# Kernel tuning notes

Measured on AMD Instinct MI355X. Metric: run time of the kernel, lower is better.

Reference implementation:

```python
import jax, jax.numpy as jnp
import numpy as np

N, F, T, C = 20000, 4, 12, 256
HID, OUT = 128, 12
ER, E = 30000, 320000


def _gcn_agg(xw, src, dst, w):
    """GCNConv propagation with self-loops (weight 1): D^-1/2 (A+I) D^-1/2 @ xw.
    xw: [N, T, C] pre-projected features; src/dst: [E] int; w: [E] edge weights."""
    n = xw.shape[0]
    deg = jnp.zeros((n,), xw.dtype).at[dst].add(w) + 1.0  # +1 from self-loop
    dinv = jax.lax.rsqrt(deg)
    coef = (dinv[src] * w * dinv[dst])[:, None, None]      # [E,1,1]
    out = jnp.zeros_like(xw).at[dst].add(coef * xw[src])   # scatter-add messages
    return out + (dinv * dinv)[:, None, None] * xw         # self-loop term


def _regional_conv(x, Wc, bc, regs):
    # Shared GCNConv applied to each of the 5 state graphs, outputs summed.
    xw = jnp.einsum("nft,fc->ntc", x, Wc)  # [N, T, C], all periods at once
    out = bc
    for (src, dst, w) in regs:
        out = out + _gcn_agg(xw, src, dst, w)
    return out


def _forward(x, attrs, idxs, Wc_z, bc_z, Wl_z, bl_z, Wc_h, bc_h, Wl_h, bl_h,
             attention, W1, b1, W2, b2):
    regs = [(idx[0], idx[1], w) for idx, w in zip(idxs, attrs)]
    # A3TGCN runs an independent TGCN-GRU step per period from H=None (zeros),
    # then attention-averages over periods. With H=0:
    #   Z = sigmoid(linear_z([conv_z(X_t), 0]))   (hidden half of Wl drops out)
    #   reset gate R multiplies H=0, so it has no effect on the output
    #   H_tilde = tanh(linear_h([conv_h(X_t), 0]));  H_t = (1-Z)*H_tilde
    cz = _regional_conv(x, Wc_z, bc_z, regs)         # [N, T, C]
    Z = jax.nn.sigmoid(cz @ Wl_z[:C] + bl_z)
    ch = _regional_conv(x, Wc_h, bc_h, regs)
    Htilde = jnp.tanh(ch @ Wl_h[:C] + bl_h)
    Ht = (1.0 - Z) * Htilde                          # [N, T, C]
    probs = jax.nn.softmax(attention)                # [T]
    h = jnp.einsum("ntc,t->nc", Ht, probs)           # temporal attention pooling
    y = jax.nn.relu(h)
    y = jax.nn.relu(y @ W1 + b1)
    y = y @ W2 + b2
    return y, h


def setup_inputs():
    key = jax.random.key(0)
    ks = jax.random.split(key, 32)
    s = 0.05
    inp = {
        "x": jax.random.normal(ks[0], (N, F, T), jnp.float32),
        "edge_index": jax.random.randint(ks[1], (2, E), 0, N, jnp.int32),
    }
    regions = ["IA", "KS", "KY", "OH", "WI"]
    for i, nm in enumerate(regions):
        inp[nm + "edge_index"] = jax.random.randint(ks[2 + i], (2, ER), 0, N, jnp.int32)
    for i, nm in enumerate(regions):
        inp[nm + "edge_attr"] = jax.random.uniform(ks[7 + i], (ER,), jnp.float32)
    for gi, g in enumerate(["z", "r", "h"]):
        inp["Wc_" + g] = jax.random.normal(ks[12 + gi], (F, C), jnp.float32) * s
        inp["bc_" + g] = jnp.zeros((C,), jnp.float32)
        inp["Wl_" + g] = jax.random.normal(ks[15 + gi], (2 * C, C), jnp.float32) * s
        inp["bl_" + g] = jnp.zeros((C,), jnp.float32)
    inp["attention"] = jax.random.normal(ks[18], (T,), jnp.float32)
    inp["W1"] = jax.random.normal(ks[19], (C, HID), jnp.float32) * s
    inp["b1"] = jnp.zeros((HID,), jnp.float32)
    inp["W2"] = jax.random.normal(ks[20], (HID, OUT), jnp.float32) * s
    inp["b2"] = jnp.zeros((OUT,), jnp.float32)
    return inp


def reference(x, edge_index, IAedge_index, KSedge_index, KYedge_index, OHedge_index, WIedge_index,
              IAedge_attr, KSedge_attr, KYedge_attr, OHedge_attr, WIedge_attr,
              Wc_z, bc_z, Wl_z, bl_z, Wc_r, bc_r, Wl_r, bl_r, Wc_h, bc_h, Wl_h, bl_h,
              attention, W1, b1, W2, b2):
    # The full-graph edge_index and the reset-gate parameters are carried by the
    # original module but cannot influence the output (regional convs use the 5
    # state graphs; the reset gate multiplies the zero initial hidden state).
    idxs = [IAedge_index, KSedge_index, KYedge_index, OHedge_index, WIedge_index]
    attrs = [IAedge_attr, KSedge_attr, KYedge_attr, OHedge_attr, WIedge_attr]
    return _forward(x, attrs, idxs, Wc_z, bc_z, Wl_z, bl_z, Wc_h, bc_h, Wl_h, bl_h,
                    attention, W1, b1, W2, b2)
```

## Files before the change

### kernel.cpp

```cpp
#include <hip/hip_runtime.h>

constexpr int N    = 20000;
constexpr int T    = 12;
constexpr int C    = 256;
constexpr int HIDN = 128;
constexpr int OUTD = 12;
constexpr int ER   = 30000;
constexpr int NFT  = 48;
constexpr int EDGE_TOT = 5 * ER;
constexpr int CAP      = 32;
constexpr int EB       = 586;

constexpr int WS_DEG    = 0;
constexpr int WS_CNT    = 100000;
constexpr int WS_MV     = 120000;
constexpr int WS_ZEND   = 122576;
constexpr int WS_WP     = 122576;
constexpr int WS_W2T    = 138960;
constexpr int WS_BUCKET = 140496;

constexpr float LOG2E = 1.4426950408889634f;

typedef __attribute__((ext_vector_type(8))) short short8;
typedef __attribute__((ext_vector_type(4))) float floatx4;
typedef __attribute__((ext_vector_type(2))) float floatx2;

#if __has_builtin(__builtin_amdgcn_exp2f)
#define EXP2(x) __builtin_amdgcn_exp2f(x)
#else
#define EXP2(x) exp2f(x)
#endif

__device__ __forceinline__ floatx2 pk_fma(floatx2 a, floatx2 b, floatx2 c) {
  floatx2 r;
  r.x = fmaf(a.x, b.x, c.x);
  r.y = fmaf(a.y, b.y, c.y);
  return r;
}

__device__ __forceinline__ short f2bf(float f) {
  unsigned u = __float_as_uint(f);
  u = u + 0x7fffu + ((u >> 16) & 1u);
  return (short)(u >> 16);
}

__device__ __forceinline__ void pick_region(
    int r,
    const int* e0, const int* e1, const int* e2, const int* e3, const int* e4,
    const float* a0, const float* a1, const float* a2, const float* a3, const float* a4,
    const int*& ei, const float*& ea) {
  switch (r) {
    case 0: ei = e0; ea = a0; break;
    case 1: ei = e1; ea = a1; break;
    case 2: ei = e2; ea = a2; break;
    case 3: ei = e3; ea = a3; break;
    default: ei = e4; ea = a4; break;
  }
}

__global__ void k_prep(
    const float* __restrict__ Wc_z, const float* __restrict__ bc_z,
    const float* __restrict__ Wl_z, const float* __restrict__ bl_z,
    const float* __restrict__ Wc_h, const float* __restrict__ bc_h,
    const float* __restrict__ Wl_h, const float* __restrict__ bl_h,
    const float* __restrict__ att, const float* __restrict__ W1,
    const float* __restrict__ W2,
    const int* __restrict__ e0, const int* __restrict__ e1,
    const int* __restrict__ e2, const int* __restrict__ e3,
    const int* __restrict__ e4,
    const float* __restrict__ a0, const float* __restrict__ a1,
    const float* __restrict__ a2, const float* __restrict__ a3,
    const float* __restrict__ a4,
    float* __restrict__ Mv, short* __restrict__ Wp, float* __restrict__ W2t,
    float* __restrict__ deg, int* __restrict__ cnt, int2* __restrict__ bucket) {
  int b = blockIdx.x, tid = threadIdx.x;
  if (b < 16) {
    int g  = b >> 3;
    int ch = b & 7;
    int k  = tid;
    const float* Wc = g ? Wc_h : Wc_z;
    const float* bc = g ? bc_h : bc_z;
    const float* Wl = g ? Wl_h : Wl_z;
    const float* bl = g ? bl_h : bl_z;
    float scale = g ? 2.0f * LOG2E : LOG2E;
    float m0 = 0.f, m1 = 0.f, m2 = 0.f, m3 = 0.f;
    float v = (ch == 0) ? bl[k] : 0.0f;
    int c0 = ch * 32;
    for (int c = c0; c < c0 + 32; c++) {
      float wl = Wl[c * C + k];
      m0 = fmaf(Wc[0 * C + c], wl, m0);
      m1 = fmaf(Wc[1 * C + c], wl, m1);
      m2 = fmaf(Wc[2 * C + c], wl, m2);
      m3 = fmaf(Wc[3 * C + c], wl, m3);
      v  = fmaf(bc[c], wl, v);
    }
    float* o = Mv + g * (5 * C);
    atomicAdd(&o[0 * C + k], scale * m0);
    atomicAdd(&o[1 * C + k], scale * m1);
    atomicAdd(&o[2 * C + k], scale * m2);
    atomicAdd(&o[3 * C + k], scale * m3);
    atomicAdd(&o[4 * C + k], scale * v);
    return;
  }
  if (b == 16) {
    if (tid < T) {
      float amax = -3.0e38f;
      for (int t = 0; t < T; t++) amax = fmaxf(amax, att[t]);
      float s = 0.f;
      for (int t = 0; t < T; t++) s += __expf(att[t] - amax);
      Mv[10 * C + tid] = __expf(att[tid] - amax) / s;
    }
    return;
  }
  if (b < 152) {
    int idx = (b - 17) * 256 + tid;
    if (idx < 32768) {
      int j    = idx & 7;
      int lane = (idx >> 3) & 63;
      int ch   = (idx >> 9) & 7;
      int kt   = idx >> 12;
      int cin  = ch * 32 + (lane >> 4) * 8 + j;
      int kout = kt * 16 + (lane & 15);
      Wp[idx] = f2bf(W1[cin * HIDN + kout]);
    } else if (idx < 32768 + 1536) {
      int r = idx - 32768;
      int o = r >> 7, k = r & 127;
      W2t[r] = W2[k * OUTD + o];
    }
    return;
  }
  int i = (b - 152) * 256 + tid;
  if (i >= EDGE_TOT) return;
  int r = i / ER;
  int e = i - r * ER;
  const int* ei; const float* ea;
  pick_region(r, e0, e1, e2, e3, e4, a0, a1, a2, a3, a4, ei, ea);
  int src = ei[e];
  int dst = ei[ER + e];
  float w = ea[e];
  atomicAdd(&deg[r * N + dst], w);
  int slot = atomicAdd(&cnt[dst], 1);
  if (slot < CAP) bucket[dst * CAP + slot] = make_int2(src | (r << 15), __float_as_int(w));
}

__global__ __launch_bounds__(256) void k_fused(
    const float* __restrict__ x, const float* __restrict__ deg,
    const int* __restrict__ cnt, const int2* __restrict__ bucket,
    const float* __restrict__ Mv, const short* __restrict__ Wp,
    const float* __restrict__ b1, const float* __restrict__ W2t,
    const float* __restrict__ b2,
    float* __restrict__ y_out, float* __restrict__ h_out) {
  __shared__ float xs[16][NFT];
  __shared__ short hs[16][264];
  __shared__ float y1s[16][132];
  int tid = threadIdx.x;
  int wave = tid >> 6, lane = tid & 63;
  int n0 = blockIdx.x * 16;

  {
    int q = lane < NFT ? lane : NFT - 1;
    int sl = lane & (CAP - 1);
    int nb = n0 + wave * 4;
    int4 cv4 = *(const int4*)&cnt[nb];
    int cvs[4] = {cv4.x, cv4.y, cv4.z, cv4.w};
    int2 mrs[4];
#pragma unroll
    for (int nl = 0; nl < 4; nl++) mrs[nl] = bucket[(nb + nl) * CAP + sl];

#pragma unroll
    for (int nl = 0; nl < 4; nl++) {
      int rl = wave * 4 + nl;
      int n = nb + nl;
      float dd0 = rsqrtf(deg[0 * N + n] + 1.0f);
      float dd1 = rsqrtf(deg[1 * N + n] + 1.0f);
      float dd2 = rsqrtf(deg[2 * N + n] + 1.0f);
      float dd3 = rsqrtf(deg[3 * N + n] + 1.0f);
      float dd4 = rsqrtf(deg[4 * N + n] + 1.0f);
      float s = dd0 * dd0 + dd1 * dd1 + dd2 * dd2 + dd3 * dd3 + dd4 * dd4;
      float facc = s * x[n * NFT + q];

      int cv = cvs[nl];
      if (cv > CAP) cv = CAP;
      int2 m  = mrs[nl];
      bool valid = sl < cv;
      int key  = valid ? m.x : 0;
      int srcv = key & 0x7fff;
      int rr   = key >> 15;
      float dsrc = deg[rr * N + srcv];
      float ddn = rr == 0 ? dd0 : rr == 1 ? dd1 : rr == 2 ? dd2
                : rr == 3 ? dd3 : dd4;
      float cf = valid ? rsqrtf(dsrc + 1.0f) * __int_as_float(m.y) * ddn : 0.0f;

      float f1 = 0.f, f2 = 0.f, f3 = 0.f;
      int cvr = (cv + 3) & ~3;
      for (int j = 0; j < cvr; j += 4) {
        int s0 = __shfl(srcv, j);
        int s1 = __shfl(srcv, j + 1);
        int s2 = __shfl(srcv, j + 2);
        int s3 = __shfl(srcv, j + 3);
        float c0 = __shfl(cf, j);
        float c1 = __shfl(cf, j + 1);
        float c2 = __shfl(cf, j + 2);
        float c3 = __shfl(cf, j + 3);
        float x0 = x[s0 * NFT + q];
        float x1 = x[s1 * NFT + q];
        float x2 = x[s2 * NFT + q];
        float x3 = x[s3 * NFT + q];
        facc = fmaf(c0, x0, facc);
        f1 = fmaf(c1, x1, f1);
        f2 = fmaf(c2, x2, f2);
        f3 = fmaf(c3, x3, f3);
      }
      facc = (facc + f1) + (f2 + f3);
      if (lane < NFT) xs[rl][lane] = facc;
    }
  }
  __syncthreads();

  {
    int half = wave & 1;
    int nb   = (wave >> 1) * 8;
    int c0 = half * 128 + (lane << 1);
    const float* Mz = Mv;
    const float* Mh = Mv + 5 * C;
    floatx2 mz[4], mh[4], vz, vh;
#pragma unroll
    for (int f = 0; f < 4; f++) {
      mz[f] = *(const floatx2*)(Mz + f * C + c0);
      mh[f] = *(const floatx2*)(Mh + f * C + c0);
    }
    vz = *(const floatx2*)(Mz + 4 * C + c0);
    vh = *(const floatx2*)(Mh + 4 * C + c0);

#pragma unroll
    for (int nl = 0; nl < 8; nl++) {
      int rl = nb + nl;
      int n = n0 + rl;
      const float* xr = &xs[rl][0];
      floatx2 acc = {0.f, 0.f};
#pragma unroll
      for (int tb = 0; tb < 3; tb++) {
        float4 xf0 = *(const float4*)(xr + 0 * T + tb * 4);
        float4 xf1 = *(const float4*)(xr + 1 * T + tb * 4);
        float4 xf2 = *(const float4*)(xr + 2 * T + tb * 4);
        float4 xf3 = *(const float4*)(xr + 3 * T + tb * 4);
        float xs0[4] = {xf0.x, xf0.y, xf0.z, xf0.w};
        float xs1[4] = {xf1.x, xf1.y, xf1.z, xf1.w};
        float xs2[4] = {xf2.x, xf2.y, xf2.z, xf2.w};
        float xs3[4] = {xf3.x, xf3.y, xf3.z, xf3.w};
#pragma unroll
        for (int tt = 0; tt < 4; tt++) {
          int t = tb * 4 + tt;
          float p = Mv[10 * C + t];
          floatx2 x0 = {xs0[tt], xs0[tt]};
          floatx2 x1 = {xs1[tt], xs1[tt]};
          floatx2 x2 = {xs2[tt], xs2[tt]};
          floatx2 x3 = {xs3[tt], xs3[tt]};
          floatx2 az = pk_fma(mz[0], x0, pk_fma(mz[1], x1, pk_fma(mz[2], x2, pk_fma(mz[3], x3, vz))));
          floatx2 ah = pk_fma(mh[0], x0, pk_fma(mh[1], x1, pk_fma(mh[2], x2, pk_fma(mh[3], x3, vh))));
          floatx2 e1, e2;
          e1.x = EXP2(az.x); e1.y = EXP2(az.y);
          e2.x = EXP2(ah.x); e2.y = EXP2(ah.y);
          floatx2 one = {1.f, 1.f};
          floatx2 d1 = e1 + one;
          floatx2 d2 = e2 + one;
          floatx2 rD;
          rD.x = __builtin_amdgcn_rcpf(d1.x * d2.x);
          rD.y = __builtin_amdgcn_rcpf(d1.y * d2.y);
          floatx2 pv = {p, p};
          floatx2 pn = pk_fma(pv, e2, -pv);
          acc = pk_fma(pn, rD, acc);
        }
      }
      float2 o = {acc.x, acc.y};
      *(float2*)(h_out + n * C + c0) = o;
      unsigned pk = (unsigned short)f2bf(fmaxf(acc.x, 0.f)) |
                    ((unsigned)(unsigned short)f2bf(fmaxf(acc.y, 0.f)) << 16);
      *(unsigned*)&hs[rl][c0] = pk;
    }
  }
  __syncthreads();

  {
    int quad = lane >> 4, col = lane & 15;
    floatx4 acc2[2];
    acc2[0] = {0.f, 0.f, 0.f, 0.f};
    acc2[1] = {0.f, 0.f, 0.f, 0.f};
#pragma unroll
    for (int ch = 0; ch < 8; ch++) {
      short8 a = *(const short8*)&hs[col][ch * 32 + quad * 8];
#pragma unroll
      for (int kk = 0; kk < 2; kk++) {
        short8 bb = ((const short8*)Wp)[((wave * 2 + kk) * 8 + ch) * 64 + lane];
        acc2[kk] = __builtin_amdgcn_mfma_f32_16x16x32_bf16(a, bb, acc2[kk], 0, 0, 0);
      }
    }
#pragma unroll
    for (int kk = 0; kk < 2; kk++) {
      int kt = wave * 2 + kk;
      float bias = b1[kt * 16 + col];
#pragma unroll
      for (int r = 0; r < 4; r++)
        y1s[quad * 4 + r][kt * 16 + col] = fmaxf(acc2[kk][r] + bias, 0.f);
    }
  }
  __syncthreads();

  if (tid < 16 * OUTD) {
    int nl = tid / OUTD, o = tid - nl * OUTD;
    float sacc = b2[o];
    const float* yr = &y1s[nl][0];
    const float* wr = W2t + o * HIDN;
#pragma unroll 8
    for (int k4 = 0; k4 < 32; k4++) {
      float4 yv = *(const float4*)(yr + 4 * k4);
      float4 wv = *(const float4*)(wr + 4 * k4);
      sacc = fmaf(yv.x, wv.x, fmaf(yv.y, wv.y, fmaf(yv.z, wv.z, fmaf(yv.w, wv.w, sacc))));
    }
    y_out[(n0 + nl) * OUTD + o] = sacc;
  }
}

extern "C" void kernel_launch(void* const* d_in, const int* in_sizes, int n_in,
                              void* d_out, int out_size, void* d_ws, size_t ws_size,
                              hipStream_t stream) {
  const float* x   = (const float*)d_in[0];
  const int* eIA = (const int*)d_in[2];
  const int* eKS = (const int*)d_in[3];
  const int* eKY = (const int*)d_in[4];
  const int* eOH = (const int*)d_in[5];
  const int* eWI = (const int*)d_in[6];
  const float* aIA = (const float*)d_in[7];
  const float* aKS = (const float*)d_in[8];
  const float* aKY = (const float*)d_in[9];
  const float* aOH = (const float*)d_in[10];
  const float* aWI = (const float*)d_in[11];
  const float* Wc_z = (const float*)d_in[12];
  const float* bc_z = (const float*)d_in[13];
  const float* Wl_z = (const float*)d_in[14];
  const float* bl_z = (const float*)d_in[15];
  const float* Wc_h = (const float*)d_in[20];
  const float* bc_h = (const float*)d_in[21];
  const float* Wl_h = (const float*)d_in[22];
  const float* bl_h = (const float*)d_in[23];
  const float* att  = (const float*)d_in[24];
  const float* W1   = (const float*)d_in[25];
  const float* b1   = (const float*)d_in[26];
  const float* W2   = (const float*)d_in[27];
  const float* b2   = (const float*)d_in[28];

  float* ws     = (float*)d_ws;
  float* deg    = ws + WS_DEG;
  int*   cnt    = (int*)(ws + WS_CNT);
  float* Mv     = ws + WS_MV;
  short* Wp     = (short*)(ws + WS_WP);
  float* W2t    = ws + WS_W2T;
  int2*  bucket = (int2*)(ws + WS_BUCKET);

  float* y_out = (float*)d_out;
  float* h_out = y_out + N * OUTD;

  hipMemsetAsync(deg, 0, WS_ZEND * sizeof(float), stream);

  k_prep<<<152 + EB, 256, 0, stream>>>(Wc_z, bc_z, Wl_z, bl_z,
                                       Wc_h, bc_h, Wl_h, bl_h,
                                       att, W1, W2,
                                       eIA, eKS, eKY, eOH, eWI,
                                       aIA, aKS, aKY, aOH, aWI,
                                       Mv, Wp, W2t, deg, cnt, bucket);
  k_fused<<<N / 16, 256, 0, stream>>>(x, deg, cnt, bucket, Mv, Wp, b1, W2t, b2,
                                      y_out, h_out);
}
```

Before: 180.1 us.

## Merge memset, prep and fused kernels into one persistent kernel with grid barriers

Replaces the memset plus two kernel launches with a single persistent kernel of 1024 blocks. Blocks zero the workspace, hit a software grid barrier, run the prep work, hit a second barrier, then loop over node tiles. The gather loop is also reworked to interleave the four nodes of each wave, with readfirstlane on the neighbour counts, to expose more memory parallelism. This removes launch gaps and kernel boundaries at the cost of spin-wait barriers, which assume all 1024 blocks are co-resident, and fewer blocks for the main phase.

```diff
diff --git a/kernel.cpp b/kernel.cpp
--- a/kernel.cpp
+++ b/kernel.cpp
@@ -10,6 +10,9 @@
 constexpr int EDGE_TOT = 5 * ER;
 constexpr int CAP      = 32;
 constexpr int EB       = 586;
+constexpr int PREP_B   = 152 + EB;
+constexpr int NT       = N / 16;
+constexpr int GRID     = 1024;
 
 constexpr int WS_DEG    = 0;
 constexpr int WS_CNT    = 100000;
@@ -58,7 +61,22 @@
   }
 }
 
-__global__ void k_prep(
+__device__ unsigned g_bar[2];
+
+__device__ __forceinline__ void grid_barrier(int which) {
+  __syncthreads();
+  if (threadIdx.x == 0) {
+    unsigned v = __hip_atomic_fetch_add(&g_bar[which], 1u,
+                                        __ATOMIC_ACQ_REL, __HIP_MEMORY_SCOPE_AGENT);
+    unsigned target = (v & ~(unsigned)(GRID - 1)) + (unsigned)GRID;
+    while (__hip_atomic_load(&g_bar[which], __ATOMIC_ACQUIRE,
+                             __HIP_MEMORY_SCOPE_AGENT) < target)
+      __builtin_amdgcn_s_sleep(1);
+  }
+  __syncthreads();
+}
+
+__global__ __launch_bounds__(256, 4) void k_all(
     const float* __restrict__ Wc_z, const float* __restrict__ bc_z,
     const float* __restrict__ Wl_z, const float* __restrict__ bl_z,
     const float* __restrict__ Wc_h, const float* __restrict__ bc_h,
@@ -71,9 +89,23 @@
     const float* __restrict__ a0, const float* __restrict__ a1,
     const float* __restrict__ a2, const float* __restrict__ a3,
     const float* __restrict__ a4,
+    const float* __restrict__ x, const float* __restrict__ b1,
+    const float* __restrict__ b2,
     float* __restrict__ Mv, short* __restrict__ Wp, float* __restrict__ W2t,
-    float* __restrict__ deg, int* __restrict__ cnt, int2* __restrict__ bucket) {
+    float* __restrict__ deg, int* __restrict__ cnt, int2* __restrict__ bucket,
+    float* __restrict__ y_out, float* __restrict__ h_out) {
+  __shared__ float xs[16][NFT];
+  __shared__ short hs[16][264];
+  __shared__ float y1s[16][132];
+
   int b = blockIdx.x, tid = threadIdx.x;
+
+  {
+    int gz = b * 256 + tid;
+    if (gz < WS_ZEND) deg[gz] = 0.0f;
+  }
+  grid_barrier(0);
+
   if (b < 16) {
     int g  = b >> 3;
     int ch = b & 7;
@@ -100,9 +132,7 @@
     atomicAdd(&o[2 * C + k], scale * m2);
     atomicAdd(&o[3 * C + k], scale * m3);
     atomicAdd(&o[4 * C + k], scale * v);
-    return;
-  }
-  if (b == 16) {
+  } else if (b == 16) {
     if (tid < T) {
       float amax = -3.0e38f;
       for (int t = 0; t < T; t++) amax = fmaxf(amax, att[t]);
@@ -110,9 +140,7 @@
       for (int t = 0; t < T; t++) s += __expf(att[t] - amax);
       Mv[10 * C + tid] = __expf(att[tid] - amax) / s;
     }
-    return;
-  }
-  if (b < 152) {
+  } else if (b < 152) {
     int idx = (b - 17) * 256 + tid;
     if (idx < 32768) {
       int j    = idx & 7;
@@ -127,197 +155,211 @@
       int o = r >> 7, k = r & 127;
       W2t[r] = W2[k * OUTD + o];
     }
-    return;
+  } else if (b < PREP_B) {
+    int i = (b - 152) * 256 + tid;
+    if (i < EDGE_TOT) {
+      int r = i / ER;
+      int e = i - r * ER;
+      const int* ei; const float* ea;
+      pick_region(r, e0, e1, e2, e3, e4, a0, a1, a2, a3, a4, ei, ea);
+      int src = ei[e];
+      int dst = ei[ER + e];
+      float w = ea[e];
+      atomicAdd(&deg[r * N + dst], w);
+      int slot = atomicAdd(&cnt[dst], 1);
+      if (slot < CAP) bucket[dst * CAP + slot] = make_int2(src | (r << 15), __float_as_int(w));
+    }
   }
-  int i = (b - 152) * 256 + tid;
-  if (i >= EDGE_TOT) return;
-  int r = i / ER;
-  int e = i - r * ER;
-  const int* ei; const float* ea;
-  pick_region(r, e0, e1, e2, e3, e4, a0, a1, a2, a3, a4, ei, ea);
-  int src = ei[e];
-  int dst = ei[ER + e];
-  float w = ea[e];
-  atomicAdd(&deg[r * N + dst], w);
-  int slot = atomicAdd(&cnt[dst], 1);
-  if (slot < CAP) bucket[dst * CAP + slot] = make_int2(src | (r << 15), __float_as_int(w));
-}
-
-__global__ __launch_bounds__(256) void k_fused(
-    const float* __restrict__ x, const float* __restrict__ deg,
-    const int* __restrict__ cnt, const int2* __restrict__ bucket,
-    const float* __restrict__ Mv, const short* __restrict__ Wp,
-    const float* __restrict__ b1, const float* __restrict__ W2t,
-    const float* __restrict__ b2,
-    float* __restrict__ y_out, float* __restrict__ h_out) {
-  __shared__ float xs[16][NFT];
-  __shared__ short hs[16][264];
-  __shared__ float y1s[16][132];
-  int tid = threadIdx.x;
+  grid_barrier(1);
+
   int wave = tid >> 6, lane = tid & 63;
-  int n0 = blockIdx.x * 16;
-
-  {
-    int q = lane < NFT ? lane : NFT - 1;
-    int sl = lane & (CAP - 1);
-    int nb = n0 + wave * 4;
-    int4 cv4 = *(const int4*)&cnt[nb];
-    int cvs[4] = {cv4.x, cv4.y, cv4.z, cv4.w};
-    int2 mrs[4];
-#pragma unroll
-    for (int nl = 0; nl < 4; nl++) mrs[nl] = bucket[(nb + nl) * CAP + sl];
-
-#pragma unroll
-    for (int nl = 0; nl < 4; nl++) {
-      int rl = wave * 4 + nl;
-      int n = nb + nl;
-      float dd0 = rsqrtf(deg[0 * N + n] + 1.0f);
-      float dd1 = rsqrtf(deg[1 * N + n] + 1.0f);
-      float dd2 = rsqrtf(deg[2 * N + n] + 1.0f);
-      float dd3 = rsqrtf(deg[3 * N + n] + 1.0f);
-      float dd4 = rsqrtf(deg[4 * N + n] + 1.0f);
-      float s = dd0 * dd0 + dd1 * dd1 + dd2 * dd2 + dd3 * dd3 + dd4 * dd4;
-      float facc = s * x[n * NFT + q];
-
-      int cv = cvs[nl];
-      if (cv > CAP) cv = CAP;
-      int2 m  = mrs[nl];
-      bool valid = sl < cv;
-      int key  = valid ? m.x : 0;
-      int srcv = key & 0x7fff;
-      int rr   = key >> 15;
-      float dsrc = deg[rr * N + srcv];
-      float ddn = rr == 0 ? dd0 : rr == 1 ? dd1 : rr == 2 ? dd2
-                : rr == 3 ? dd3 : dd4;
-      float cf = valid ? rsqrtf(dsrc + 1.0f) * __int_as_float(m.y) * ddn : 0.0f;
-
-      float f1 = 0.f, f2 = 0.f, f3 = 0.f;
-      int cvr = (cv + 3) & ~3;
-      for (int j = 0; j < cvr; j += 4) {
-        int s0 = __shfl(srcv, j);
-        int s1 = __shfl(srcv, j + 1);
-        int s2 = __shfl(srcv, j + 2);
-        int s3 = __shfl(srcv, j + 3);
-        float c0 = __shfl(cf, j);
-        float c1 = __shfl(cf, j + 1);
-        float c2 = __shfl(cf, j + 2);
-        float c3 = __shfl(cf, j + 3);
-        float x0 = x[s0 * NFT + q];
-        float x1 = x[s1 * NFT + q];
-        float x2 = x[s2 * NFT + q];
-        float x3 = x[s3 * NFT + q];
-        facc = fmaf(c0, x0, facc);
-        f1 = fmaf(c1, x1, f1);
-        f2 = fmaf(c2, x2, f2);
-        f3 = fmaf(c3, x3, f3);
-      }
-      facc = (facc + f1) + (f2 + f3);
-      if (lane < NFT) xs[rl][lane] = facc;
-    }
-  }
-  __syncthreads();
-
-  {
-    int half = wave & 1;
-    int nb   = (wave >> 1) * 8;
-    int c0 = half * 128 + (lane << 1);
-    const float* Mz = Mv;
-    const float* Mh = Mv + 5 * C;
-    floatx2 mz[4], mh[4], vz, vh;
-#pragma unroll
-    for (int f = 0; f < 4; f++) {
-      mz[f] = *(const floatx2*)(Mz + f * C + c0);
-      mh[f] = *(const floatx2*)(Mh + f * C + c0);
-    }
-    vz = *(const floatx2*)(Mz + 4 * C + c0);
-    vh = *(const floatx2*)(Mh + 4 * C + c0);
-
-#pragma unroll
-    for (int nl = 0; nl < 8; nl++) {
-      int rl = nb + nl;
-      int n = n0 + rl;
-      const float* xr = &xs[rl][0];
-      floatx2 acc = {0.f, 0.f};
-#pragma unroll
-      for (int tb = 0; tb < 3; tb++) {
-        float4 xf0 = *(const float4*)(xr + 0 * T + tb * 4);
-        float4 xf1 = *(const float4*)(xr + 1 * T + tb * 4);
-        float4 xf2 = *(const float4*)(xr + 2 * T + tb * 4);
-        float4 xf3 = *(const float4*)(xr + 3 * T + tb * 4);
-        float xs0[4] = {xf0.x, xf0.y, xf0.z, xf0.w};
-        float xs1[4] = {xf1.x, xf1.y, xf1.z, xf1.w};
-        float xs2[4] = {xf2.x, xf2.y, xf2.z, xf2.w};
-        float xs3[4] = {xf3.x, xf3.y, xf3.z, xf3.w};
-#pragma unroll
-        for (int tt = 0; tt < 4; tt++) {
-          int t = tb * 4 + tt;
-          float p = Mv[10 * C + t];
-          floatx2 x0 = {xs0[tt], xs0[tt]};
-          floatx2 x1 = {xs1[tt], xs1[tt]};
-          floatx2 x2 = {xs2[tt], xs2[tt]};
-          floatx2 x3 = {xs3[tt], xs3[tt]};
-          floatx2 az = pk_fma(mz[0], x0, pk_fma(mz[1], x1, pk_fma(mz[2], x2, pk_fma(mz[3], x3, vz))));
-          floatx2 ah = pk_fma(mh[0], x0, pk_fma(mh[1], x1, pk_fma(mh[2], x2, pk_fma(mh[3], x3, vh))));
-          floatx2 e1, e2;
-          e1.x = EXP2(az.x); e1.y = EXP2(az.y);
-          e2.x = EXP2(ah.x); e2.y = EXP2(ah.y);
-          floatx2 one = {1.f, 1.f};
-          floatx2 d1 = e1 + one;
-          floatx2 d2 = e2 + one;
-          floatx2 rD;
-          rD.x = __builtin_amdgcn_rcpf(d1.x * d2.x);
-          rD.y = __builtin_amdgcn_rcpf(d1.y * d2.y);
-          floatx2 pv = {p, p};
-          floatx2 pn = pk_fma(pv, e2, -pv);
-          acc = pk_fma(pn, rD, acc);
+
+  for (int tile = b; tile < NT; tile += GRID) {
+    int n0 = tile * 16;
+
+    {
+      int q = lane < NFT ? lane : NFT - 1;
+      int sl = lane & (CAP - 1);
+      int nb = n0 + wave * 4;
+      int4 cv4 = *(const int4*)&cnt[nb];
+      int cvs[4];
+      cvs[0] = __builtin_amdgcn_readfirstlane(cv4.x);
+      cvs[1] = __builtin_amdgcn_readfirstlane(cv4.y);
+      cvs[2] = __builtin_amdgcn_readfirstlane(cv4.z);
+      cvs[3] = __builtin_amdgcn_readfirstlane(cv4.w);
+#pragma unroll
+      for (int nl = 0; nl < 4; nl++) cvs[nl] = cvs[nl] > CAP ? CAP : cvs[nl];
+
+      int2 mrs[4];
+#pragma unroll
+      for (int nl = 0; nl < 4; nl++) mrs[nl] = bucket[(nb + nl) * CAP + sl];
+
+      int srcs[4]; float cfs[4];
+      float fa[4], fb[4], fc[4], fd[4];
+#pragma unroll
+      for (int nl = 0; nl < 4; nl++) {
+        int n = nb + nl;
+        float dd0 = rsqrtf(deg[0 * N + n] + 1.0f);
+        float dd1 = rsqrtf(deg[1 * N + n] + 1.0f);
+        float dd2 = rsqrtf(deg[2 * N + n] + 1.0f);
+        float dd3 = rsqrtf(deg[3 * N + n] + 1.0f);
+        float dd4 = rsqrtf(deg[4 * N + n] + 1.0f);
+        float s = dd0 * dd0 + dd1 * dd1 + dd2 * dd2 + dd3 * dd3 + dd4 * dd4;
+        fa[nl] = s * x[n * NFT + q];
+        fb[nl] = 0.f; fc[nl] = 0.f; fd[nl] = 0.f;
+
+        bool valid = sl < cvs[nl];
+        int key  = valid ? mrs[nl].x : 0;
+        int srcv = key & 0x7fff;
+        int rr   = key >> 15;
+        float dsrc = deg[rr * N + srcv];
+        float ddn = rr == 0 ? dd0 : rr == 1 ? dd1 : rr == 2 ? dd2
+                  : rr == 3 ? dd3 : dd4;
+        cfs[nl]  = valid ? rsqrtf(dsrc + 1.0f) * __int_as_float(mrs[nl].y) * ddn : 0.0f;
+        srcs[nl] = srcv;
+      }
+
+      int cvr0 = (cvs[0] + 3) & ~3, cvr1 = (cvs[1] + 3) & ~3;
+      int cvr2 = (cvs[2] + 3) & ~3, cvr3 = (cvs[3] + 3) & ~3;
+      int cvm01 = cvr0 > cvr1 ? cvr0 : cvr1;
+      int cvm23 = cvr2 > cvr3 ? cvr2 : cvr3;
+      int cvm = cvm01 > cvm23 ? cvm01 : cvm23;
+      int cvr[4] = {cvr0, cvr1, cvr2, cvr3};
+
+      for (int j = 0; j < cvm; j += 4) {
+#pragma unroll
+        for (int nl = 0; nl < 4; nl++) {
+          if (j < cvr[nl]) {
+            int s0 = __shfl(srcs[nl], j);
+            int s1 = __shfl(srcs[nl], j + 1);
+            int s2 = __shfl(srcs[nl], j + 2);
+            int s3 = __shfl(srcs[nl], j + 3);
+            float c0 = __shfl(cfs[nl], j);
+            float c1 = __shfl(cfs[nl], j + 1);
+            float c2 = __shfl(cfs[nl], j + 2);
+            float c3 = __shfl(cfs[nl], j + 3);
+            float x0 = x[s0 * NFT + q];
+            float x1 = x[s1 * NFT + q];
+            float x2 = x[s2 * NFT + q];
+            float x3 = x[s3 * NFT + q];
+            fa[nl] = fmaf(c0, x0, fa[nl]);
+            fb[nl] = fmaf(c1, x1, fb[nl]);
+            fc[nl] = fmaf(c2, x2, fc[nl]);
+            fd[nl] = fmaf(c3, x3, fd[nl]);
+          }
         }
       }
-      float2 o = {acc.x, acc.y};
-      *(float2*)(h_out + n * C + c0) = o;
-      unsigned pk = (unsigned short)f2bf(fmaxf(acc.x, 0.f)) |
-                    ((unsigned)(unsigned short)f2bf(fmaxf(acc.y, 0.f)) << 16);
-      *(unsigned*)&hs[rl][c0] = pk;
-    }
-  }
-  __syncthreads();
-
-  {
-    int quad = lane >> 4, col = lane & 15;
-    floatx4 acc2[2];
-    acc2[0] = {0.f, 0.f, 0.f, 0.f};
-    acc2[1] = {0.f, 0.f, 0.f, 0.f};
-#pragma unroll
-    for (int ch = 0; ch < 8; ch++) {
-      short8 a = *(const short8*)&hs[col][ch * 32 + quad * 8];
+#pragma unroll
+      for (int nl = 0; nl < 4; nl++) {
+        float facc = (fa[nl] + fb[nl]) + (fc[nl] + fd[nl]);
+        if (lane < NFT) xs[wave * 4 + nl][lane] = facc;
+      }
+    }
+    __syncthreads();
+
+    {
+      int half = wave & 1;
+      int nb   = (wave >> 1) * 8;
+      int c0 = half * 128 + (lane << 1);
+      const float* Mz = Mv;
+      const float* Mh = Mv + 5 * C;
+      floatx2 mz[4], mh[4], vz, vh;
+#pragma unroll
+      for (int f = 0; f < 4; f++) {
+        mz[f] = *(const floatx2*)(Mz + f * C + c0);
+        mh[f] = *(const floatx2*)(Mh + f * C + c0);
+      }
+      vz = *(const floatx2*)(Mz + 4 * C + c0);
+      vh = *(const floatx2*)(Mh + 4 * C + c0);
+
+#pragma unroll
+      for (int nl = 0; nl < 8; nl++) {
+        int rl = nb + nl;
+        int n = n0 + rl;
+        const float* xr = &xs[rl][0];
+        floatx2 acc = {0.f, 0.f};
+#pragma unroll
+        for (int tb = 0; tb < 3; tb++) {
+          float4 xf0 = *(const float4*)(xr + 0 * T + tb * 4);
+          float4 xf1 = *(const float4*)(xr + 1 * T + tb * 4);
+          float4 xf2 = *(const float4*)(xr + 2 * T + tb * 4);
+          float4 xf3 = *(const float4*)(xr + 3 * T + tb * 4);
+          float xs0[4] = {xf0.x, xf0.y, xf0.z, xf0.w};
+          float xs1[4] = {xf1.x, xf1.y, xf1.z, xf1.w};
+          float xs2[4] = {xf2.x, xf2.y, xf2.z, xf2.w};
+          float xs3[4] = {xf3.x, xf3.y, xf3.z, xf3.w};
+#pragma unroll
+          for (int tt = 0; tt < 4; tt++) {
+            int t = tb * 4 + tt;
+            float p = Mv[10 * C + t];
+            floatx2 x0 = {xs0[tt], xs0[tt]};
+            floatx2 x1 = {xs1[tt], xs1[tt]};
+            floatx2 x2 = {xs2[tt], xs2[tt]};
+            floatx2 x3 = {xs3[tt], xs3[tt]};
+            floatx2 az = pk_fma(mz[0], x0, pk_fma(mz[1], x1, pk_fma(mz[2], x2, pk_fma(mz[3], x3, vz))));
+            floatx2 ah = pk_fma(mh[0], x0, pk_fma(mh[1], x1, pk_fma(mh[2], x2, pk_fma(mh[3], x3, vh))));
+            floatx2 e1, e2;
+            e1.x = EXP2(az.x); e1.y = EXP2(az.y);
+            e2.x = EXP2(ah.x); e2.y = EXP2(ah.y);
+            floatx2 one = {1.f, 1.f};
+            floatx2 d1 = e1 + one;
+            floatx2 d2 = e2 + one;
+            floatx2 rD;
+            rD.x = __builtin_amdgcn_rcpf(d1.x * d2.x);
+            rD.y = __builtin_amdgcn_rcpf(d1.y * d2.y);
+            floatx2 pv = {p, p};
+            floatx2 pn = pk_fma(pv, e2, -pv);
+            acc = pk_fma(pn, rD, acc);
+          }
+        }
+        float2 o = {acc.x, acc.y};
+        *(float2*)(h_out + n * C + c0) = o;
+        unsigned pk = (unsigned short)f2bf(fmaxf(acc.x, 0.f)) |
+                      ((unsigned)(unsigned short)f2bf(fmaxf(acc.y, 0.f)) << 16);
+        *(unsigned*)&hs[rl][c0] = pk;
+      }
+    }
+    __syncthreads();
+
+    {
+      int quad = lane >> 4, col = lane & 15;
+      floatx4 acc2[2];
+      acc2[0] = {0.f, 0.f, 0.f, 0.f};
+      acc2[1] = {0.f, 0.f, 0.f, 0.f};
+#pragma unroll
+      for (int ch = 0; ch < 8; ch++) {
+        short8 a = *(const short8*)&hs[col][ch * 32 + quad * 8];
+#pragma unroll
+        for (int kk = 0; kk < 2; kk++) {
+          short8 bb = ((const short8*)Wp)[((wave * 2 + kk) * 8 + ch) * 64 + lane];
+          acc2[kk] = __builtin_amdgcn_mfma_f32_16x16x32_bf16(a, bb, acc2[kk], 0, 0, 0);
+        }
+      }
 #pragma unroll
       for (int kk = 0; kk < 2; kk++) {
-        short8 bb = ((const short8*)Wp)[((wave * 2 + kk) * 8 + ch) * 64 + lane];
-        acc2[kk] = __builtin_amdgcn_mfma_f32_16x16x32_bf16(a, bb, acc2[kk], 0, 0, 0);
-      }
-    }
-#pragma unroll
-    for (int kk = 0; kk < 2; kk++) {
-      int kt = wave * 2 + kk;
-      float bias = b1[kt * 16 + col];
-#pragma unroll
-      for (int r = 0; r < 4; r++)
-        y1s[quad * 4 + r][kt * 16 + col] = fmaxf(acc2[kk][r] + bias, 0.f);
-    }
-  }
-  __syncthreads();
-
-  if (tid < 16 * OUTD) {
-    int nl = tid / OUTD, o = tid - nl * OUTD;
-    float sacc = b2[o];
-    const float* yr = &y1s[nl][0];
-    const float* wr = W2t + o * HIDN;
+        int kt = wave * 2 + kk;
+        float bias = b1[kt * 16 + col];
+#pragma unroll
+        for (int r = 0; r < 4; r++)
+          y1s[quad * 4 + r][kt * 16 + col] = fmaxf(acc2[kk][r] + bias, 0.f);
+      }
+    }
+    __syncthreads();
+
+    if (tid < 16 * OUTD) {
+      int nl = tid / OUTD, o = tid - nl * OUTD;
+      float sacc = b2[o];
+      const float* yr = &y1s[nl][0];
+      const float* wr = W2t + o * HIDN;
 #pragma unroll 8
-    for (int k4 = 0; k4 < 32; k4++) {
-      float4 yv = *(const float4*)(yr + 4 * k4);
-      float4 wv = *(const float4*)(wr + 4 * k4);
-      sacc = fmaf(yv.x, wv.x, fmaf(yv.y, wv.y, fmaf(yv.z, wv.z, fmaf(yv.w, wv.w, sacc))));
-    }
-    y_out[(n0 + nl) * OUTD + o] = sacc;
+      for (int k4 = 0; k4 < 32; k4++) {
+        float4 yv = *(const float4*)(yr + 4 * k4);
+        float4 wv = *(const float4*)(wr + 4 * k4);
+        sacc = fmaf(yv.x, wv.x, fmaf(yv.y, wv.y, fmaf(yv.z, wv.z, fmaf(yv.w, wv.w, sacc))));
+      }
+      y_out[(n0 + nl) * OUTD + o] = sacc;
+    }
+    __syncthreads();
   }
 }
 
@@ -360,14 +402,13 @@
   float* y_out = (float*)d_out;
   float* h_out = y_out + N * OUTD;
 
-  hipMemsetAsync(deg, 0, WS_ZEND * sizeof(float), stream);
-
-  k_prep<<<152 + EB, 256, 0, stream>>>(Wc_z, bc_z, Wl_z, bl_z,
-                                       Wc_h, bc_h, Wl_h, bl_h,
-                                       att, W1, W2,
-                                       eIA, eKS, eKY, eOH, eWI,
-                                       aIA, aKS, aKY, aOH, aWI,
-                                       Mv, Wp, W2t, deg, cnt, bucket);
-  k_fused<<<N / 16, 256, 0, stream>>>(x, deg, cnt, bucket, Mv, Wp, b1, W2t, b2,
-                                      y_out, h_out);
-}
+  k_all<<<GRID, 256, 0, stream>>>(Wc_z, bc_z, Wl_z, bl_z,
+                                  Wc_h, bc_h, Wl_h, bl_h,
+                                  att, W1, W2,
+                                  eIA, eKS, eKY, eOH, eWI,
+                                  aIA, aKS, aKY, aOH, aWI,
+                                  x, b1, b2,
+                                  Mv, Wp, W2t,
+                                  deg, cnt, bucket,
+                                  y_out, h_out);
+}
```

New measurement: 317.7 us. +76.5%, slower.
